# Performance work log

Hardware: AMD Instinct MI355X
Metric: run time of the kernel (lower is better)

The kernel has to match this reference:

```python
import jax, jax.numpy as jnp
import numpy as np

N, E, F_IN, E_IN, HID, H, C, L, OUT = 20000, 320000, 128, 64, 64, 4, 64, 4, 32


def setup_inputs() -> dict:
    key = jax.random.key(0)
    ks = jax.random.split(key, 24)
    s = 0.05
    return {
        'x': jax.random.normal(ks[0], (N, F_IN), jnp.float32),
        'edge_index': jax.random.randint(ks[1], (2, E), 0, N, jnp.int32),
        'edge_attr': jax.random.normal(ks[2], (E, E_IN), jnp.float32),
        'node_W': jax.random.normal(ks[3], (F_IN, HID), jnp.float32) * s,
        'node_b': jnp.zeros((HID,), jnp.float32),
        'eenc_W': jax.random.normal(ks[4], (E_IN, HID), jnp.float32) * s,
        'eenc_b': jnp.zeros((HID,), jnp.float32),
        'Wq': jax.random.normal(ks[5], (L, HID, H * C), jnp.float32) * s,
        'bq': jnp.zeros((L, H * C), jnp.float32),
        'Wk': jax.random.normal(ks[6], (L, HID, H * C), jnp.float32) * s,
        'bk': jnp.zeros((L, H * C), jnp.float32),
        'Wv': jax.random.normal(ks[7], (L, HID, H * C), jnp.float32) * s,
        'bv': jnp.zeros((L, H * C), jnp.float32),
        'We': jax.random.normal(ks[8], (L, HID, H * C), jnp.float32) * s,  # lin_edge, bias=False in PyG
        'Wskip': jax.random.normal(ks[9], (L, HID, HID), jnp.float32) * s,
        'bskip': jnp.zeros((L, HID), jnp.float32),
        'ln_g': jnp.ones((L, HID), jnp.float32),
        'ln_b': jnp.zeros((L, HID), jnp.float32),
        'lin_W': jax.random.normal(ks[10], (HID, OUT), jnp.float32) * s,
        'lin_b': jnp.zeros((OUT,), jnp.float32),
    }


def _layernorm(h, g, b):
    mu = h.mean(-1, keepdims=True)
    var = ((h - mu) ** 2).mean(-1, keepdims=True)
    return (h - mu) * jax.lax.rsqrt(var + 1e-5) * g + b


def _transformer_conv(h, ea, src, dst, Wq, bq, Wk, bk, Wv, bv, We, Wskip, bskip):
    n = h.shape[0]
    q = (h @ Wq + bq).reshape(n, H, C)[dst]          # [E,H,C] dst (x_i)
    k = (h @ Wk + bk).reshape(n, H, C)[src]          # [E,H,C] src (x_j)
    v = (h @ Wv + bv).reshape(n, H, C)[src]
    e = (ea @ We).reshape(-1, H, C)                  # per-edge features
    k = k + e
    alpha = (q * k).sum(-1) * (1.0 / jnp.sqrt(jnp.float32(C)))   # [E,H]
    amax = jax.ops.segment_max(alpha, dst, num_segments=n)       # segment softmax over dst
    ex = jnp.exp(alpha - amax[dst])
    denom = jax.ops.segment_sum(ex, dst, num_segments=n)
    a = ex / (denom[dst] + 1e-16)
    msg = (v + e) * a[..., None]                     # [E,H,C]
    out = jax.ops.segment_sum(msg, dst, num_segments=n)          # [N,H,C]
    out = out.mean(axis=1)                           # concat=False -> head mean
    return out + (h @ Wskip + bskip)                 # root_weight skip


def reference(x, edge_index, edge_attr, node_W, node_b, eenc_W, eenc_b,
              Wq, bq, Wk, bk, Wv, bv, We, Wskip, bskip, ln_g, ln_b, lin_W, lin_b):
    src, dst = edge_index[0], edge_index[1]
    h = x @ node_W + node_b
    ea = edge_attr @ eenc_W + eenc_b
    # layer 0: conv only (per the forward body)
    h = _transformer_conv(h, ea, src, dst, Wq[0], bq[0], Wk[0], bk[0], Wv[0], bv[0],
                          We[0], Wskip[0], bskip[0])
    # layers 1..L-1: res+ block (norm -> relu -> [dropout=id at eval] -> conv -> +res)
    for l in range(1, L):
        res = h
        z = _layernorm(h, ln_g[l], ln_b[l])
        z = jax.nn.relu(z)
        z = _transformer_conv(z, ea, src, dst, Wq[l], bq[l], Wk[l], bk[l], Wv[l], bv[l],
                              We[l], Wskip[l], bskip[l])
        h = z + res
    h = _layernorm(h, ln_g[0], ln_b[0])
    h = jax.nn.relu(h)
    return h @ lin_W + lin_b
```

## Files before the change

kernel.cpp:

```cpp
#include <hip/hip_runtime.h>
#include <hip/hip_fp16.h>
#include <math.h>

#define N_NODES 20000
#define N_EDGES 320000
#define F_IN    128
#define E_IN    64
#define HID     64
#define NH      4
#define CH      64
#define HC      256
#define L_LAYERS 4
#define OUT_DIM 32
#define WCOLS   1088

typedef _Float16 half8 __attribute__((ext_vector_type(8)));
typedef float f32x4 __attribute__((ext_vector_type(4)));

__global__ __launch_bounds__(256) void node_enc(const float* __restrict__ x,
                                                const float* __restrict__ W,
                                                const float* __restrict__ b,
                                                float* __restrict__ h) {
    int base_node = blockIdx.x * 4;
    int t = threadIdx.x;
    __shared__ float xs[4][F_IN];
    for (int i = t; i < 4 * F_IN; i += 256) {
        int nn = base_node + i / F_IN;
        xs[i / F_IN][i % F_IN] = (nn < N_NODES) ? x[nn * F_IN + (i % F_IN)] : 0.f;
    }
    __syncthreads();
    int node = base_node + t / 64;
    int col  = t & 63;
    if (node >= N_NODES) return;
    float acc = b[col];
    const float* xr = xs[t / 64];
    for (int i = 0; i < F_IN; i++) acc += xr[i] * W[i * HID + col];
    h[node * HID + col] = acc;
}

__global__ __launch_bounds__(256) void hist_dst(const int* __restrict__ dst,
                                                int* __restrict__ hist) {
    int e = blockIdx.x * 256 + threadIdx.x;
    if (e < N_EDGES) atomicAdd(&hist[dst[e]], 1);
}

__global__ __launch_bounds__(256) void bin_hist(const int* __restrict__ hist,
                                                int* __restrict__ bins) {
    int n = blockIdx.x * 256 + threadIdx.x;
    if (n >= N_NODES) return;
    int d = hist[n]; if (d > 255) d = 255;
    atomicAdd(&bins[d], 1);
}

__global__ __launch_bounds__(256) void scan_bins(const int* __restrict__ bins,
                                                 int* __restrict__ curb) {
    __shared__ int s[256];
    int t = threadIdx.x;
    s[t] = bins[t];
    __syncthreads();
    int acc = 0;
    for (int b = t + 1; b < 256; b++) acc += s[b];
    curb[t] = acc;
}

__global__ __launch_bounds__(256) void assign_rank(const int* __restrict__ hist,
                                                   int* __restrict__ curb,
                                                   int* __restrict__ node_order,
                                                   int* __restrict__ rank_of,
                                                   int* __restrict__ deg_rank) {
    int n = blockIdx.x * 256 + threadIdx.x;
    if (n >= N_NODES) return;
    int d = hist[n];
    int b = d > 255 ? 255 : d;
    int r = atomicAdd(&curb[b], 1);
    node_order[r] = n;
    rank_of[n] = r;
    deg_rank[r] = d;
}

__global__ __launch_bounds__(1024) void scan_hist(const int* __restrict__ arr,
                                                  int* __restrict__ row_ptr,
                                                  int* __restrict__ cursor) {
    __shared__ int sums[1024];
    const int CHUNK = 20;
    int t = threadIdx.x;
    int base = t * CHUNK;
    int local[CHUNK];
    int s = 0;
    for (int i = 0; i < CHUNK; i++) {
        int idx = base + i;
        int vv = (idx < N_NODES) ? arr[idx] : 0;
        local[i] = s;
        s += vv;
    }
    sums[t] = s;
    __syncthreads();
    for (int off = 1; off < 1024; off <<= 1) {
        int v = (t >= off) ? sums[t - off] : 0;
        __syncthreads();
        sums[t] += v;
        __syncthreads();
    }
    int excl = (t == 0) ? 0 : sums[t - 1];
    for (int i = 0; i < CHUNK; i++) {
        int idx = base + i;
        if (idx < N_NODES) {
            int p = excl + local[i];
            row_ptr[idx] = p;
            cursor[idx] = p;
        }
    }
    if (t == 1023) row_ptr[N_NODES] = sums[1023];
}

__global__ __launch_bounds__(256) void compute_pos(const int* __restrict__ src,
                                                   const int* __restrict__ dst,
                                                   const int* __restrict__ rank_of,
                                                   int* __restrict__ cursor2,
                                                   int* __restrict__ eid_of,
                                                   int* __restrict__ srcrank_perm) {
    int e = blockIdx.x * 256 + threadIdx.x;
    if (e >= N_EDGES) return;
    int r = rank_of[dst[e]];
    int pos = atomicAdd(&cursor2[r], 1);
    eid_of[pos] = e;
    srcrank_perm[pos] = rank_of[src[e]];
}

__global__ __launch_bounds__(256) void permute_attr(const int* __restrict__ eid_of,
                                                    const float* __restrict__ eattr,
                                                    __half* __restrict__ attr_p) {
    int t = threadIdx.x;
    int wave = t >> 6, lane = t & 63;
    int p = blockIdx.x * 16 + wave * 4 + (lane >> 4);
    if (p >= N_EDGES) return;
    int e = eid_of[p];
    int qi = (lane & 15) * 4;
    float4 a = *(const float4*)(eattr + (size_t)e * E_IN + qi);
    __half2 h0 = __floats2half2_rn(a.x, a.y);
    __half2 h1 = __floats2half2_rn(a.z, a.w);
    uint2 packed;
    packed.x = *(unsigned int*)&h0;
    packed.y = *(unsigned int*)&h1;
    *(uint2*)(attr_p + (size_t)p * E_IN + qi) = packed;
}

__global__ __launch_bounds__(256) void make_wqe(const float* __restrict__ Wq,
                                                const float* __restrict__ bq,
                                                const float* __restrict__ We,
                                                float* __restrict__ Wqe,
                                                float* __restrict__ bqe) {
    int l = blockIdx.x / HID;
    int i = blockIdx.x % HID;
    int t = threadIdx.x;
    int h = t >> 6, j = t & 63;
    const float* WqL = Wq + (size_t)l * HID * HC;
    const float* WeL = We + (size_t)l * HID * HC;
    float acc = 0.f;
    for (int c = 0; c < CH; c++)
        acc += WqL[i * HC + h * CH + c] * WeL[j * HC + h * CH + c];
    Wqe[(size_t)l * HID * HC + i * HC + t] = acc;
    if (i == 0) {
        const float* bqL = bq + l * HC;
        float accb = 0.f;
        for (int c = 0; c < CH; c++)
            accb += bqL[h * CH + c] * WeL[j * HC + h * CH + c];
        bqe[l * HC + t] = accb;
    }
}

__global__ __launch_bounds__(256) void make_wqe2(const float* __restrict__ Wqe,
                                                 const float* __restrict__ bqe,
                                                 const float* __restrict__ eW,
                                                 const float* __restrict__ eb,
                                                 float* __restrict__ Wqe2,
                                                 float* __restrict__ bqe2,
                                                 float* __restrict__ wqb,
                                                 float* __restrict__ bqb) {
    int l = blockIdx.x / HID, i = blockIdx.x % HID;
    int t = threadIdx.x;
    int h2 = t >> 6, m = t & 63;
    const float* Wr = Wqe + (size_t)l * HID * HC + i * HC + h2 * CH;
    float acc = 0.f;
    for (int j = 0; j < HID; j++) acc += Wr[j] * eW[m * HID + j];
    Wqe2[(size_t)l * HID * HC + i * HC + t] = acc;
    if (m == 0) {
        float a = 0.f;
        for (int j = 0; j < HID; j++) a += Wr[j] * eb[j];
        wqb[l * HID * NH + i * NH + h2] = a;
    }
    if (i == 0) {
        const float* br = bqe + l * HC + h2 * CH;
        float a = 0.f;
        for (int j = 0; j < HID; j++) a += br[j] * eW[m * HID + j];
        bqe2[l * HC + t] = a;
        if (m == 0) {
            float bb = 0.f;
            for (int j = 0; j < HID; j++) bb += br[j] * eb[j];
            bqb[l * NH + h2] = bb;
        }
    }
}

__global__ __launch_bounds__(256) void make_weE16(const float* __restrict__ eW,
                                                  const float* __restrict__ eb,
                                                  const float* __restrict__ We,
                                                  _Float16* __restrict__ WeE16T,
                                                  float* __restrict__ beE) {
    int l = blockIdx.x / E_IN, m = blockIdx.x % E_IN;
    int t = threadIdx.x;
    const float* WeL = We + (size_t)l * HID * HC;
    float acc = 0.f;
    for (int j = 0; j < HID; j++) acc += eW[m * HID + j] * WeL[j * HC + t];
    WeE16T[((size_t)l * HC + t) * 64 + m] = (_Float16)acc;
    if (m == 0) {
        float a = 0.f;
        for (int j = 0; j < HID; j++) a += eb[j] * WeL[j * HC + t];
        beE[l * HC + t] = a;
    }
}

__global__ __launch_bounds__(256) void make_w16(
        const float* __restrict__ Wq, const float* __restrict__ Wk,
        const float* __restrict__ Wv, const float* __restrict__ Wqe2,
        const float* __restrict__ Wsk,
        const float* __restrict__ bq, const float* __restrict__ bk,
        const float* __restrict__ bv, const float* __restrict__ bqe2,
        const float* __restrict__ bsk,
        _Float16* __restrict__ W16T, float* __restrict__ biasc) {
    int l = blockIdx.x / 272;
    int cg = blockIdx.x % 272;
    int col = cg * 4 + (threadIdx.x >> 6);
    int i = threadIdx.x & 63;
    float w, b;
    if (col < 256)       { w = Wq[(size_t)l*HID*HC + i*HC + col];          b = bq[l*HC + col]; }
    else if (col < 512)  { w = Wk[(size_t)l*HID*HC + i*HC + col-256];      b = bk[l*HC + col-256]; }
    else if (col < 768)  { w = Wv[(size_t)l*HID*HC + i*HC + col-512];      b = bv[l*HC + col-512]; }
    else if (col < 1024) { w = Wqe2[(size_t)l*HID*HC + i*HC + col-768];    b = bqe2[l*HC + col-768]; }
    else                 { w = Wsk[(size_t)l*HID*HID + i*HID + col-1024];  b = bsk[l*HID + col-1024]; }
    W16T[((size_t)l * WCOLS + col) * 64 + i] = (_Float16)w;
    if (i == 0) biasc[l * WCOLS + col] = b;
}

__global__ __launch_bounds__(256) void node_pre0(const float* __restrict__ h,
        const int* __restrict__ node_order,
        const _Float16* __restrict__ W16T, const float* __restrict__ biasc,
        const float* __restrict__ wqb, const float* __restrict__ bqb,
        _Float16* __restrict__ qqw, _Float16* __restrict__ kv,
        float* __restrict__ skip, float* __restrict__ qb) {
    int t = threadIdx.x;
    int wave = t >> 6, lane = t & 63;
    int base = blockIdx.x * 32;
    __shared__ _Float16 zs[32][72];
    __shared__ int nord[32];
    if (t < 32) nord[t] = node_order[base + t];
    __syncthreads();
    for (int it = 0; it < 8; it++) {
        int m = it * 4 + wave;
        zs[m][lane] = (_Float16)h[nord[m] * HID + lane];
    }
    __syncthreads();
    if (t < 128) {
        int m = t >> 2, h4 = t & 3;
        float a = bqb[h4];
        for (int i = 0; i < HID; i++) a += (float)zs[m][i] * wqb[i * NH + h4];
        qb[(base + m) * NH + h4] = a;
    }
    int quad = lane >> 4;
    int mrow = lane & 15;
    half8 a00 = *(const half8*)&zs[mrow][quad * 8];
    half8 a01 = *(const half8*)&zs[mrow][32 + quad * 8];
    half8 a10 = *(const half8*)&zs[16 + mrow][quad * 8];
    half8 a11 = *(const half8*)&zs[16 + mrow][32 + quad * 8];
    int colwave = wave * 272;
    for (int tile = 0; tile < 17; tile++) {
        int colb = colwave + tile * 16;
        int col = colb + mrow;
        const _Float16* wrow = W16T + (size_t)col * 64;
        half8 b0 = *(const half8*)(wrow + quad * 8);
        half8 b1 = *(const half8*)(wrow + 32 + quad * 8);
        f32x4 acc0 = {0.f, 0.f, 0.f, 0.f};
        f32x4 acc1 = {0.f, 0.f, 0.f, 0.f};
        acc0 = __builtin_amdgcn_mfma_f32_16x16x32_f16(a00, b0, acc0, 0, 0, 0);
        acc0 = __builtin_amdgcn_mfma_f32_16x16x32_f16(a01, b1, acc0, 0, 0, 0);
        acc1 = __builtin_amdgcn_mfma_f32_16x16x32_f16(a10, b0, acc1, 0, 0, 0);
        acc1 = __builtin_amdgcn_mfma_f32_16x16x32_f16(a11, b1, acc1, 0, 0, 0);
        float bi = biasc[col];
        int seg = colb >> 8;
        int r0 = base + quad * 4;
#pragma unroll
        for (int reg = 0; reg < 4; reg++) {
            float v0 = acc0[reg] + bi;
            float v1 = acc1[reg] + bi;
            int ra = r0 + reg, rb = ra + 16;
            if (seg == 0) {
                int p = (col >> 2) * 8 + (col & 3);
                qqw[(size_t)ra * 512 + p] = (_Float16)v0;
                qqw[(size_t)rb * 512 + p] = (_Float16)v1;
            } else if (seg == 1) {
                int c = col - 256, kp = (c >> 2) * 8 + (c & 3);
                kv[(size_t)ra * 512 + kp] = (_Float16)v0;
                kv[(size_t)rb * 512 + kp] = (_Float16)v1;
            } else if (seg == 2) {
                int c = col - 512, kp = (c >> 2) * 8 + 4 + (c & 3);
                kv[(size_t)ra * 512 + kp] = (_Float16)v0;
                kv[(size_t)rb * 512 + kp] = (_Float16)v1;
            } else if (seg == 3) {
                int c = col - 768, p = (c >> 2) * 8 + 4 + (c & 3);
                qqw[(size_t)ra * 512 + p] = (_Float16)v0;
                qqw[(size_t)rb * 512 + p] = (_Float16)v1;
            } else {
                int c = col - 1024;
                skip[ra * HID + c] = v0;
                skip[rb * HID + c] = v1;
            }
        }
    }
}

__global__ __launch_bounds__(256) void gather_edges(
        const int* __restrict__ new_rp,
        const int* __restrict__ srcrank_perm, const __half* __restrict__ attr_p,
        const __half* __restrict__ kv,
        const float* __restrict__ qb,
        const __half* qqw,
        float* numv, __half* __restrict__ numea16,
        float* __restrict__ den) {
    int wave = threadIdx.x >> 6;
    int lane = threadIdx.x & 63;
    int r = blockIdx.x * 4 + wave;
    if (r >= N_NODES) return;
    int e0 = new_rp[r], e1 = new_rp[r + 1];
    int qi = (lane & 15) * 4;
    int head = lane >> 4;
    uint4 qr = *(const uint4*)(qqw + (size_t)r * 512 + lane * 8);
    float2 q01 = __half22float2(*(__half2*)&qr.x);
    float2 q23 = __half22float2(*(__half2*)&qr.y);
    float2 w01 = __half22float2(*(__half2*)&qr.z);
    float2 w23 = __half22float2(*(__half2*)&qr.w);
    float qbh = qb[r * NH + head];
    float4 nv = make_float4(0.f, 0.f, 0.f, 0.f);
    float4 ne = make_float4(0.f, 0.f, 0.f, 0.f);
    float dsum = 0.f;
#pragma unroll 2
    for (int e = e0; e < e1; e++) {
        int s_ = srcrank_perm[e];
        uint2 araw = *(const uint2*)(attr_p + (size_t)e * E_IN + qi);
        uint4 kraw = *(const uint4*)(kv + (size_t)s_ * (2 * HC) + lane * 8);
        float2 a01 = __half22float2(*(__half2*)&araw.x);
        float2 a23 = __half22float2(*(__half2*)&araw.y);
        float2 k01 = __half22float2(*(__half2*)&kraw.x);
        float2 k23 = __half22float2(*(__half2*)&kraw.y);
        float2 v01 = __half22float2(*(__half2*)&kraw.z);
        float2 v23 = __half22float2(*(__half2*)&kraw.w);
        float rr = q01.x * k01.x + q01.y * k01.y + q23.x * k23.x + q23.y * k23.y
                 + w01.x * a01.x + w01.y * a01.y + w23.x * a23.x + w23.y * a23.y;
        rr += __shfl_xor(rr, 1);
        rr += __shfl_xor(rr, 2);
        rr += __shfl_xor(rr, 4);
        rr += __shfl_xor(rr, 8);
        float ex = __expf((rr + qbh) * 0.125f);
        nv.x += ex * v01.x; nv.y += ex * v01.y; nv.z += ex * v23.x; nv.w += ex * v23.y;
        ne.x += ex * a01.x; ne.y += ex * a01.y; ne.z += ex * a23.x; ne.w += ex * a23.y;
        dsum += ex;
    }
    *(float4*)(numv + (size_t)r * HC + lane * 4) = nv;
    __half2 n01 = __floats2half2_rn(ne.x, ne.y);
    __half2 n23 = __floats2half2_rn(ne.z, ne.w);
    uint2 np;
    np.x = *(unsigned int*)&n01;
    np.y = *(unsigned int*)&n23;
    *(uint2*)(numea16 + (size_t)r * HC + lane * 4) = np;
    if ((lane & 15) == 0) den[r * NH + head] = dsum;
}

__global__ __launch_bounds__(256) void node_mid(
        const int* __restrict__ node_order,
        const float* numv,
        const __half* __restrict__ numea16,
        const float* __restrict__ den_g,
        float* skip,
        float* __restrict__ h,
        const _Float16* __restrict__ WeE16T,
        const float* __restrict__ beE,
        int add_res,
        const _Float16* __restrict__ W16T,
        const float* __restrict__ biasc,
        const float* __restrict__ wqb, const float* __restrict__ bqb,
        const float* __restrict__ g, const float* __restrict__ be,
        _Float16* qqw, _Float16* __restrict__ kv,
        float* __restrict__ qb) {
    int t = threadIdx.x;
    int wave = t >> 6, lane = t & 63;
    int quad = lane >> 4, mrow = lane & 15;
    int base = blockIdx.x * 16;
    __shared__ _Float16 ea16[16][264];
    __shared__ float hsum[4][16][64];
    __shared__ float hnew[16][64];
    __shared__ _Float16 zs[16][72];
    __shared__ float bsh[256];
    __shared__ float dsh[64];
    __shared__ int nord[16];
    if (t < 16) nord[t] = node_order[base + t];
    if (t < 64) dsh[t] = den_g[base * 4 + t];
    bsh[t] = beE[t];
    for (int it = 0; it < 2; it++) {
        int idx = it * 256 + t;
        int m = idx >> 5, c8 = idx & 31;
        uint4 raw = *(const uint4*)(numea16 + (size_t)(base + m) * HC + c8 * 8);
        *(uint4*)&ea16[m][c8 * 8] = raw;
    }
    __syncthreads();
    {
        int hd = wave;
        half8 a_lo = *(const half8*)&ea16[mrow][hd * 64 + quad * 8];
        half8 a_hi = *(const half8*)&ea16[mrow][hd * 64 + 32 + quad * 8];
        for (int nt = 0; nt < 4; nt++) {
            int c = nt * 16 + mrow;
            const _Float16* bp = WeE16T + (size_t)(hd * 64 + c) * 64;
            half8 b_lo = *(const half8*)(bp + quad * 8);
            half8 b_hi = *(const half8*)(bp + 32 + quad * 8);
            f32x4 acc = {0.f, 0.f, 0.f, 0.f};
            acc = __builtin_amdgcn_mfma_f32_16x16x32_f16(a_lo, b_lo, acc, 0, 0, 0);
            acc = __builtin_amdgcn_mfma_f32_16x16x32_f16(a_hi, b_hi, acc, 0, 0, 0);
            int tp = hd * 64 + c;
#pragma unroll
            for (int reg = 0; reg < 4; reg++) {
                int m = quad * 4 + reg;
                float nvv = numv[(size_t)(base + m) * HC + tp];
                float dd = dsh[m * 4 + hd];
                hsum[hd][m][c] = (nvv + acc[reg] + dd * bsh[tp]) / (dd + 1e-16f) * 0.25f;
            }
        }
    }
    __syncthreads();
    for (int it = 0; it < 4; it++) {
        int idx = it * 256 + t;
        int m = idx >> 6, c = idx & 63;
        float s = hsum[0][m][c] + hsum[1][m][c] + hsum[2][m][c] + hsum[3][m][c]
                + skip[(base + m) * HID + c];
        if (add_res) s += h[nord[m] * HID + c];
        h[nord[m] * HID + c] = s;
        hnew[m][c] = s;
    }
    __syncthreads();
    for (int it = 0; it < 4; it++) {
        int m = it * 4 + wave;
        float val = hnew[m][lane];
        float mu = val;
        for (int o = 32; o > 0; o >>= 1) mu += __shfl_xor(mu, o);
        mu *= (1.f / 64.f);
        float d = val - mu;
        float var = d * d;
        for (int o = 32; o > 0; o >>= 1) var += __shfl_xor(var, o);
        var *= (1.f / 64.f);
        val = fmaxf(d * rsqrtf(var + 1e-5f) * g[lane] + be[lane], 0.f);
        zs[m][lane] = (_Float16)val;
    }
    __syncthreads();
    if (t < 64) {
        int m = t >> 2, h4 = t & 3;
        float a = bqb[h4];
        for (int i = 0; i < HID; i++) a += (float)zs[m][i] * wqb[i * NH + h4];
        qb[(base + m) * NH + h4] = a;
    }
    half8 a00 = *(const half8*)&zs[mrow][quad * 8];
    half8 a01 = *(const half8*)&zs[mrow][32 + quad * 8];
    int colwave = wave * 272;
    for (int tile = 0; tile < 17; tile++) {
        int colb = colwave + tile * 16;
        int col = colb + mrow;
        const _Float16* wrow = W16T + (size_t)col * 64;
        half8 b0 = *(const half8*)(wrow + quad * 8);
        half8 b1 = *(const half8*)(wrow + 32 + quad * 8);
        f32x4 acc = {0.f, 0.f, 0.f, 0.f};
        acc = __builtin_amdgcn_mfma_f32_16x16x32_f16(a00, b0, acc, 0, 0, 0);
        acc = __builtin_amdgcn_mfma_f32_16x16x32_f16(a01, b1, acc, 0, 0, 0);
        float bi = biasc[col];
        int seg = colb >> 8;
#pragma unroll
        for (int reg = 0; reg < 4; reg++) {
            float v0 = acc[reg] + bi;
            int ra = base + quad * 4 + reg;
            if (seg == 0) {
                qqw[(size_t)ra * 512 + (col >> 2) * 8 + (col & 3)] = (_Float16)v0;
            } else if (seg == 1) {
                int c = col - 256;
                kv[(size_t)ra * 512 + (c >> 2) * 8 + (c & 3)] = (_Float16)v0;
            } else if (seg == 2) {
                int c = col - 512;
                kv[(size_t)ra * 512 + (c >> 2) * 8 + 4 + (c & 3)] = (_Float16)v0;
            } else if (seg == 3) {
                int c = col - 768;
                qqw[(size_t)ra * 512 + (c >> 2) * 8 + 4 + (c & 3)] = (_Float16)v0;
            } else {
                skip[ra * HID + (col - 1024)] = v0;
            }
        }
    }
}

__global__ __launch_bounds__(256) void node_fin(
        const int* __restrict__ node_order,
        const float* __restrict__ numv,
        const __half* __restrict__ numea16,
        const float* __restrict__ den_g,
        const float* __restrict__ skip,
        const float* __restrict__ h,
        const _Float16* __restrict__ WeE16T, const float* __restrict__ beE,
        const float* __restrict__ g, const float* __restrict__ be,
        const float* __restrict__ linW, const float* __restrict__ linb,
        float* __restrict__ out) {
    int t = threadIdx.x;
    int wave = t >> 6, lane = t & 63;
    int quad = lane >> 4, mrow = lane & 15;
    int base = blockIdx.x * 16;
    __shared__ _Float16 ea16[16][264];
    __shared__ float hsum[4][16][64];
    __shared__ float hnew[16][64];
    __shared__ float bsh[256];
    __shared__ float dsh[64];
    __shared__ int nord[16];
    if (t < 16) nord[t] = node_order[base + t];
    if (t < 64) dsh[t] = den_g[base * 4 + t];
    bsh[t] = beE[t];
    for (int it = 0; it < 2; it++) {
        int idx = it * 256 + t;
        int m = idx >> 5, c8 = idx & 31;
        uint4 raw = *(const uint4*)(numea16 + (size_t)(base + m) * HC + c8 * 8);
        *(uint4*)&ea16[m][c8 * 8] = raw;
    }
    __syncthreads();
    {
        int hd = wave;
        half8 a_lo = *(const half8*)&ea16[mrow][hd * 64 + quad * 8];
        half8 a_hi = *(const half8*)&ea16[mrow][hd * 64 + 32 + quad * 8];
        for (int nt = 0; nt < 4; nt++) {
            int c = nt * 16 + mrow;
            const _Float16* bp = WeE16T + (size_t)(hd * 64 + c) * 64;
            half8 b_lo = *(const half8*)(bp + quad * 8);
            half8 b_hi = *(const half8*)(bp + 32 + quad * 8);
            f32x4 acc = {0.f, 0.f, 0.f, 0.f};
            acc = __builtin_amdgcn_mfma_f32_16x16x32_f16(a_lo, b_lo, acc, 0, 0, 0);
            acc = __builtin_amdgcn_mfma_f32_16x16x32_f16(a_hi, b_hi, acc, 0, 0, 0);
            int tp = hd * 64 + c;
#pragma unroll
            for (int reg = 0; reg < 4; reg++) {
                int m = quad * 4 + reg;
                float nvv = numv[(size_t)(base + m) * HC + tp];
                float dd = dsh[m * 4 + hd];
                hsum[hd][m][c] = (nvv + acc[reg] + dd * bsh[tp]) / (dd + 1e-16f) * 0.25f;
            }
        }
    }
    __syncthreads();
    for (int it = 0; it < 4; it++) {
        int idx = it * 256 + t;
        int m = idx >> 6, c = idx & 63;
        float s = hsum[0][m][c] + hsum[1][m][c] + hsum[2][m][c] + hsum[3][m][c]
                + skip[(base + m) * HID + c] + h[nord[m] * HID + c];
        hnew[m][c] = s;
    }
    __syncthreads();
    for (int it = 0; it < 4; it++) {
        int m = it * 4 + wave;
        float val = hnew[m][lane];
        float mu = val;
        for (int o = 32; o > 0; o >>= 1) mu += __shfl_xor(mu, o);
        mu *= (1.f / 64.f);
        float d = val - mu;
        float var = d * d;
        for (int o = 32; o > 0; o >>= 1) var += __shfl_xor(var, o);
        var *= (1.f / 64.f);
        hnew[m][lane] = fmaxf(d * rsqrtf(var + 1e-5f) * g[lane] + be[lane], 0.f);
    }
    __syncthreads();
    for (int it = 0; it < 2; it++) {
        int idx = it * 256 + t;
        int m = idx >> 5, col = idx & 31;
        float a = linb[col];
        for (int i = 0; i < HID; i++) a += hnew[m][i] * linW[i * OUT_DIM + col];
        out[nord[m] * OUT_DIM + col] = a;
    }
}

extern "C" void kernel_launch(void* const* d_in, const int* in_sizes, int n_in,
                              void* d_out, int out_size, void* d_ws, size_t ws_size,
                              hipStream_t stream) {
    const float* x      = (const float*)d_in[0];
    const int*   ei     = (const int*)d_in[1];
    const float* eattr  = (const float*)d_in[2];
    const float* node_W = (const float*)d_in[3];
    const float* node_b = (const float*)d_in[4];
    const float* eenc_W = (const float*)d_in[5];
    const float* eenc_b = (const float*)d_in[6];
    const float* Wq     = (const float*)d_in[7];
    const float* bq     = (const float*)d_in[8];
    const float* Wk     = (const float*)d_in[9];
    const float* bk     = (const float*)d_in[10];
    const float* Wv     = (const float*)d_in[11];
    const float* bv     = (const float*)d_in[12];
    const float* We     = (const float*)d_in[13];
    const float* Wskip  = (const float*)d_in[14];
    const float* bskip  = (const float*)d_in[15];
    const float* ln_g   = (const float*)d_in[16];
    const float* ln_b   = (const float*)d_in[17];
    const float* lin_W  = (const float*)d_in[18];
    const float* lin_b  = (const float*)d_in[19];
    float* out = (float*)d_out;

    const int* src = ei;
    const int* dst = ei + N_EDGES;

    float* ws = (float*)d_ws;
    __half* attr_p = (__half*)ws; ws += (size_t)N_EDGES * E_IN / 2;
    float* Wqe    = (float*)attr_p;
    float* h    = ws; ws += N_NODES * HID;
    _Float16* qqw = (_Float16*)ws; ws += (size_t)N_NODES * HC;
    float* numv = (float*)qqw;
    __half* numea16 = (__half*)ws; ws += (size_t)N_NODES * HC / 2;
    _Float16* kv = (_Float16*)ws; ws += (size_t)N_NODES * HC;
    float* skip = ws; ws += N_NODES * HID;
    float* den  = ws; ws += N_NODES * NH;
    float* qb   = ws; ws += N_NODES * NH;
    float* bqe  = ws; ws += L_LAYERS * HC;
    float* Wqe2 = ws; ws += (size_t)L_LAYERS * HID * HC;
    float* bqe2 = ws; ws += L_LAYERS * HC;
    float* wqb  = ws; ws += L_LAYERS * HID * NH;
    float* bqb  = ws; ws += L_LAYERS * NH;
    _Float16* WeE16T = (_Float16*)ws; ws += (size_t)L_LAYERS * HC * HID / 2;
    float* beE  = ws; ws += L_LAYERS * HC;
    _Float16* W16T = (_Float16*)ws; ws += (size_t)L_LAYERS * WCOLS * HID / 2;
    float* biasc = ws; ws += L_LAYERS * WCOLS;
    int* ip = (int*)ws;
    int* hist         = ip; ip += N_NODES;
    int* bins         = ip; ip += 256;
    int* curb         = ip; ip += 256;
    int* node_order   = ip; ip += N_NODES;
    int* rank_of      = ip; ip += N_NODES;
    int* deg_rank     = ip; ip += N_NODES;
    int* new_rp       = ip; ip += N_NODES + 4;
    int* cursor2      = ip; ip += N_NODES;
    int* srcrank_perm = ip; ip += N_EDGES;
    int* eid_of       = ip; ip += N_EDGES;

    node_enc<<<(N_NODES + 3) / 4, 256, 0, stream>>>(x, node_W, node_b, h);

    hipMemsetAsync(hist, 0, N_NODES * sizeof(int), stream);
    hipMemsetAsync(bins, 0, 256 * sizeof(int), stream);
    hist_dst<<<(N_EDGES + 255) / 256, 256, 0, stream>>>(dst, hist);
    bin_hist<<<(N_NODES + 255) / 256, 256, 0, stream>>>(hist, bins);
    scan_bins<<<1, 256, 0, stream>>>(bins, curb);
    assign_rank<<<(N_NODES + 255) / 256, 256, 0, stream>>>(hist, curb, node_order,
                                                           rank_of, deg_rank);
    scan_hist<<<1, 1024, 0, stream>>>(deg_rank, new_rp, cursor2);

    make_wqe<<<L_LAYERS * HID, 256, 0, stream>>>(Wq, bq, We, Wqe, bqe);
    make_wqe2<<<L_LAYERS * HID, 256, 0, stream>>>(Wqe, bqe, eenc_W, eenc_b,
                                                  Wqe2, bqe2, wqb, bqb);
    make_weE16<<<L_LAYERS * E_IN, 256, 0, stream>>>(eenc_W, eenc_b, We, WeE16T, beE);
    make_w16<<<L_LAYERS * 272, 256, 0, stream>>>(Wq, Wk, Wv, Wqe2, Wskip,
                                                 bq, bk, bv, bqe2, bskip,
                                                 W16T, biasc);

    compute_pos<<<(N_EDGES + 255) / 256, 256, 0, stream>>>(src, dst, rank_of, cursor2,
                                                           eid_of, srcrank_perm);
    permute_attr<<<N_EDGES / 16, 256, 0, stream>>>(eid_of, eattr, attr_p);

    node_pre0<<<N_NODES / 32, 256, 0, stream>>>(
        h, node_order, W16T, biasc, wqb, bqb, qqw, kv, skip, qb);

    for (int l = 0; l < L_LAYERS; l++) {
        gather_edges<<<(N_NODES + 3) / 4, 256, 0, stream>>>(
            new_rp, srcrank_perm, attr_p, (const __half*)kv, qb,
            (const __half*)qqw, numv, numea16, den);
        if (l < L_LAYERS - 1) {
            node_mid<<<N_NODES / 16, 256, 0, stream>>>(
                node_order, numv, numea16, den, skip, h,
                WeE16T + (size_t)l * HC * HID, beE + l * HC,
                (l > 0) ? 1 : 0,
                W16T + (size_t)(l + 1) * WCOLS * HID, biasc + (l + 1) * WCOLS,
                wqb + (l + 1) * HID * NH, bqb + (l + 1) * NH,
                ln_g + (l + 1) * HID, ln_b + (l + 1) * HID,
                qqw, kv, qb);
        } else {
            node_fin<<<N_NODES / 16, 256, 0, stream>>>(
                node_order, numv, numea16, den, skip, h,
                WeE16T + (size_t)l * HC * HID, beE + l * HC,
                ln_g, ln_b, lin_W, lin_b, out);
        }
    }
}
```

Measured before the change: 811.0 us.

## Fuse setup kernels and node encoder into MFMA pre-pass, simplify weight layout

Merges the four degree-binning/ranking/scan kernels into one single-block kernel, and fuses the two weight-precomposition kernels using shared memory. The node encoder is folded into node_pre0 as an fp16 MFMA GEMM over x, which removes a kernel and the fp32 h round-trip. Weight columns are pre-interleaved in make_w16 so the epilogue stores contiguously without per-segment index math. The main costs targeted are launch overhead and extra memory passes in setup. In exchange, the single-block build_order serialises 20000 nodes on one CU, and the encoder now runs in fp16 precision.

```diff
diff --git a/kernel.cpp b/kernel.cpp
--- a/kernel.cpp
+++ b/kernel.cpp
@@ -17,79 +17,51 @@
 typedef _Float16 half8 __attribute__((ext_vector_type(8)));
 typedef float f32x4 __attribute__((ext_vector_type(4)));
 
-__global__ __launch_bounds__(256) void node_enc(const float* __restrict__ x,
-                                                const float* __restrict__ W,
-                                                const float* __restrict__ b,
-                                                float* __restrict__ h) {
-    int base_node = blockIdx.x * 4;
-    int t = threadIdx.x;
-    __shared__ float xs[4][F_IN];
-    for (int i = t; i < 4 * F_IN; i += 256) {
-        int nn = base_node + i / F_IN;
-        xs[i / F_IN][i % F_IN] = (nn < N_NODES) ? x[nn * F_IN + (i % F_IN)] : 0.f;
-    }
-    __syncthreads();
-    int node = base_node + t / 64;
-    int col  = t & 63;
-    if (node >= N_NODES) return;
-    float acc = b[col];
-    const float* xr = xs[t / 64];
-    for (int i = 0; i < F_IN; i++) acc += xr[i] * W[i * HID + col];
-    h[node * HID + col] = acc;
-}
-
 __global__ __launch_bounds__(256) void hist_dst(const int* __restrict__ dst,
                                                 int* __restrict__ hist) {
     int e = blockIdx.x * 256 + threadIdx.x;
     if (e < N_EDGES) atomicAdd(&hist[dst[e]], 1);
 }
 
-__global__ __launch_bounds__(256) void bin_hist(const int* __restrict__ hist,
-                                                int* __restrict__ bins) {
-    int n = blockIdx.x * 256 + threadIdx.x;
-    if (n >= N_NODES) return;
-    int d = hist[n]; if (d > 255) d = 255;
-    atomicAdd(&bins[d], 1);
-}
-
-__global__ __launch_bounds__(256) void scan_bins(const int* __restrict__ bins,
-                                                 int* __restrict__ curb) {
-    __shared__ int s[256];
+__global__ __launch_bounds__(1024) void build_order(const int* __restrict__ hist,
+                                                    int* __restrict__ node_order,
+                                                    int* __restrict__ rank_of,
+                                                    int* __restrict__ deg_rank,
+                                                    int* __restrict__ new_rp,
+                                                    int* __restrict__ cursor2) {
+    __shared__ int bins[256];
+    __shared__ int curb[256];
+    __shared__ int sums[1024];
     int t = threadIdx.x;
-    s[t] = bins[t];
-    __syncthreads();
-    int acc = 0;
-    for (int b = t + 1; b < 256; b++) acc += s[b];
-    curb[t] = acc;
-}
-
-__global__ __launch_bounds__(256) void assign_rank(const int* __restrict__ hist,
-                                                   int* __restrict__ curb,
-                                                   int* __restrict__ node_order,
-                                                   int* __restrict__ rank_of,
-                                                   int* __restrict__ deg_rank) {
-    int n = blockIdx.x * 256 + threadIdx.x;
-    if (n >= N_NODES) return;
-    int d = hist[n];
-    int b = d > 255 ? 255 : d;
-    int r = atomicAdd(&curb[b], 1);
-    node_order[r] = n;
-    rank_of[n] = r;
-    deg_rank[r] = d;
-}
-
-__global__ __launch_bounds__(1024) void scan_hist(const int* __restrict__ arr,
-                                                  int* __restrict__ row_ptr,
-                                                  int* __restrict__ cursor) {
-    __shared__ int sums[1024];
+    if (t < 256) bins[t] = 0;
+    __syncthreads();
+    for (int n = t; n < N_NODES; n += 1024) {
+        int d = hist[n]; if (d > 255) d = 255;
+        atomicAdd(&bins[d], 1);
+    }
+    __syncthreads();
+    if (t < 256) {
+        int acc = 0;
+        for (int b = t + 1; b < 256; b++) acc += bins[b];
+        curb[t] = acc;
+    }
+    __syncthreads();
+    for (int n = t; n < N_NODES; n += 1024) {
+        int d = hist[n];
+        int b = d > 255 ? 255 : d;
+        int r = atomicAdd(&curb[b], 1);
+        node_order[r] = n;
+        rank_of[n] = r;
+        deg_rank[r] = d;
+    }
+    __syncthreads();
     const int CHUNK = 20;
-    int t = threadIdx.x;
     int base = t * CHUNK;
     int local[CHUNK];
     int s = 0;
     for (int i = 0; i < CHUNK; i++) {
         int idx = base + i;
-        int vv = (idx < N_NODES) ? arr[idx] : 0;
+        int vv = (idx < N_NODES) ? deg_rank[idx] : 0;
         local[i] = s;
         s += vv;
     }
@@ -106,11 +78,11 @@
         int idx = base + i;
         if (idx < N_NODES) {
             int p = excl + local[i];
-            row_ptr[idx] = p;
-            cursor[idx] = p;
-        }
-    }
-    if (t == 1023) row_ptr[N_NODES] = sums[1023];
+            new_rp[idx] = p;
+            cursor2[idx] = p;
+        }
+    }
+    if (t == 1023) new_rp[N_NODES] = sums[1023];
 }
 
 __global__ __launch_bounds__(256) void compute_pos(const int* __restrict__ src,
@@ -145,32 +117,9 @@
     *(uint2*)(attr_p + (size_t)p * E_IN + qi) = packed;
 }
 
-__global__ __launch_bounds__(256) void make_wqe(const float* __restrict__ Wq,
-                                                const float* __restrict__ bq,
-                                                const float* __restrict__ We,
-                                                float* __restrict__ Wqe,
-                                                float* __restrict__ bqe) {
-    int l = blockIdx.x / HID;
-    int i = blockIdx.x % HID;
-    int t = threadIdx.x;
-    int h = t >> 6, j = t & 63;
-    const float* WqL = Wq + (size_t)l * HID * HC;
-    const float* WeL = We + (size_t)l * HID * HC;
-    float acc = 0.f;
-    for (int c = 0; c < CH; c++)
-        acc += WqL[i * HC + h * CH + c] * WeL[j * HC + h * CH + c];
-    Wqe[(size_t)l * HID * HC + i * HC + t] = acc;
-    if (i == 0) {
-        const float* bqL = bq + l * HC;
-        float accb = 0.f;
-        for (int c = 0; c < CH; c++)
-            accb += bqL[h * CH + c] * WeL[j * HC + h * CH + c];
-        bqe[l * HC + t] = accb;
-    }
-}
-
-__global__ __launch_bounds__(256) void make_wqe2(const float* __restrict__ Wqe,
-                                                 const float* __restrict__ bqe,
+__global__ __launch_bounds__(256) void make_wqeA(const float* __restrict__ Wq,
+                                                 const float* __restrict__ bq,
+                                                 const float* __restrict__ We,
                                                  const float* __restrict__ eW,
                                                  const float* __restrict__ eb,
                                                  float* __restrict__ Wqe2,
@@ -179,24 +128,39 @@
                                                  float* __restrict__ bqb) {
     int l = blockIdx.x / HID, i = blockIdx.x % HID;
     int t = threadIdx.x;
+    int h = t >> 6, j = t & 63;
+    __shared__ float wrow[256];
+    __shared__ float brow[256];
+    const float* WqL = Wq + (size_t)l * HID * HC;
+    const float* WeL = We + (size_t)l * HID * HC;
+    float acc = 0.f;
+    for (int c = 0; c < CH; c++)
+        acc += WqL[i * HC + h * CH + c] * WeL[j * HC + h * CH + c];
+    wrow[t] = acc;
+    if (i == 0) {
+        const float* bqL = bq + l * HC;
+        float ab = 0.f;
+        for (int c = 0; c < CH; c++)
+            ab += bqL[h * CH + c] * WeL[j * HC + h * CH + c];
+        brow[t] = ab;
+    }
+    __syncthreads();
     int h2 = t >> 6, m = t & 63;
-    const float* Wr = Wqe + (size_t)l * HID * HC + i * HC + h2 * CH;
-    float acc = 0.f;
-    for (int j = 0; j < HID; j++) acc += Wr[j] * eW[m * HID + j];
-    Wqe2[(size_t)l * HID * HC + i * HC + t] = acc;
+    float a2 = 0.f;
+    for (int jj = 0; jj < HID; jj++) a2 += wrow[h2 * 64 + jj] * eW[m * HID + jj];
+    Wqe2[(size_t)l * HID * HC + i * HC + t] = a2;
     if (m == 0) {
-        float a = 0.f;
-        for (int j = 0; j < HID; j++) a += Wr[j] * eb[j];
-        wqb[l * HID * NH + i * NH + h2] = a;
+        float aw = 0.f;
+        for (int jj = 0; jj < HID; jj++) aw += wrow[h2 * 64 + jj] * eb[jj];
+        wqb[l * HID * NH + i * NH + h2] = aw;
     }
     if (i == 0) {
-        const float* br = bqe + l * HC + h2 * CH;
-        float a = 0.f;
-        for (int j = 0; j < HID; j++) a += br[j] * eW[m * HID + j];
-        bqe2[l * HC + t] = a;
+        float ab2 = 0.f;
+        for (int jj = 0; jj < HID; jj++) ab2 += brow[h2 * 64 + jj] * eW[m * HID + jj];
+        bqe2[l * HC + t] = ab2;
         if (m == 0) {
             float bb = 0.f;
-            for (int j = 0; j < HID; j++) bb += br[j] * eb[j];
+            for (int jj = 0; jj < HID; jj++) bb += brow[h2 * 64 + jj] * eb[jj];
             bqb[l * NH + h2] = bb;
         }
     }
@@ -233,31 +197,77 @@
     int col = cg * 4 + (threadIdx.x >> 6);
     int i = threadIdx.x & 63;
     float w, b;
-    if (col < 256)       { w = Wq[(size_t)l*HID*HC + i*HC + col];          b = bq[l*HC + col]; }
-    else if (col < 512)  { w = Wk[(size_t)l*HID*HC + i*HC + col-256];      b = bk[l*HC + col-256]; }
-    else if (col < 768)  { w = Wv[(size_t)l*HID*HC + i*HC + col-512];      b = bv[l*HC + col-512]; }
-    else if (col < 1024) { w = Wqe2[(size_t)l*HID*HC + i*HC + col-768];    b = bqe2[l*HC + col-768]; }
-    else                 { w = Wsk[(size_t)l*HID*HID + i*HID + col-1024];  b = bsk[l*HID + col-1024]; }
+    if (col < 512) {
+        int c = (col >> 3) * 4 + (col & 3);
+        if ((col >> 2) & 1) { w = Wqe2[(size_t)l*HID*HC + i*HC + c]; b = bqe2[l*HC + c]; }
+        else                { w = Wq[(size_t)l*HID*HC + i*HC + c];   b = bq[l*HC + c]; }
+    } else if (col < 1024) {
+        int cc = col - 512;
+        int c = (cc >> 3) * 4 + (cc & 3);
+        if ((cc >> 2) & 1) { w = Wv[(size_t)l*HID*HC + i*HC + c]; b = bv[l*HC + c]; }
+        else               { w = Wk[(size_t)l*HID*HC + i*HC + c]; b = bk[l*HC + c]; }
+    } else {
+        int c = col - 1024;
+        w = Wsk[(size_t)l*HID*HID + i*HID + c];  b = bsk[l*HID + c];
+    }
     W16T[((size_t)l * WCOLS + col) * 64 + i] = (_Float16)w;
     if (i == 0) biasc[l * WCOLS + col] = b;
 }
 
-__global__ __launch_bounds__(256) void node_pre0(const float* __restrict__ h,
+__global__ __launch_bounds__(256) void make_w0(const float* __restrict__ nW,
+                                               const float* __restrict__ nb,
+                                               _Float16* __restrict__ W0T,
+                                               float* __restrict__ b0) {
+    int col = blockIdx.x * 2 + (threadIdx.x >> 7);
+    int i = threadIdx.x & 127;
+    W0T[col * F_IN + i] = (_Float16)nW[i * HID + col];
+    if (i == 0) b0[col] = nb[col];
+}
+
+__global__ __launch_bounds__(256) void node_pre0(const float* __restrict__ x,
         const int* __restrict__ node_order,
+        const _Float16* __restrict__ W0T, const float* __restrict__ b0,
         const _Float16* __restrict__ W16T, const float* __restrict__ biasc,
         const float* __restrict__ wqb, const float* __restrict__ bqb,
         _Float16* __restrict__ qqw, _Float16* __restrict__ kv,
         float* __restrict__ skip, float* __restrict__ qb) {
     int t = threadIdx.x;
     int wave = t >> 6, lane = t & 63;
+    int quad = lane >> 4, mrow = lane & 15;
     int base = blockIdx.x * 32;
+    __shared__ _Float16 xs[32][136];
     __shared__ _Float16 zs[32][72];
     __shared__ int nord[32];
     if (t < 32) nord[t] = node_order[base + t];
     __syncthreads();
-    for (int it = 0; it < 8; it++) {
-        int m = it * 4 + wave;
-        zs[m][lane] = (_Float16)h[nord[m] * HID + lane];
+    for (int it = 0; it < 4; it++) {
+        int idx = it * 256 + t;
+        int m = idx >> 5, c4 = idx & 31;
+        float4 a = *(const float4*)(x + (size_t)nord[m] * F_IN + c4 * 4);
+        _Float16* d = &xs[m][c4 * 4];
+        d[0] = (_Float16)a.x; d[1] = (_Float16)a.y;
+        d[2] = (_Float16)a.z; d[3] = (_Float16)a.w;
+    }
+    __syncthreads();
+    {
+        int col = wave * 16 + mrow;
+        const _Float16* w0row = W0T + (size_t)col * F_IN;
+        f32x4 acc0 = {0.f, 0.f, 0.f, 0.f};
+        f32x4 acc1 = {0.f, 0.f, 0.f, 0.f};
+#pragma unroll
+        for (int kk = 0; kk < 4; kk++) {
+            half8 bfrag = *(const half8*)(w0row + kk * 32 + quad * 8);
+            half8 af0 = *(const half8*)&xs[mrow][kk * 32 + quad * 8];
+            half8 af1 = *(const half8*)&xs[16 + mrow][kk * 32 + quad * 8];
+            acc0 = __builtin_amdgcn_mfma_f32_16x16x32_f16(af0, bfrag, acc0, 0, 0, 0);
+            acc1 = __builtin_amdgcn_mfma_f32_16x16x32_f16(af1, bfrag, acc1, 0, 0, 0);
+        }
+        float bb = b0[col];
+#pragma unroll
+        for (int reg = 0; reg < 4; reg++) {
+            zs[quad * 4 + reg][col] = (_Float16)(acc0[reg] + bb);
+            zs[16 + quad * 4 + reg][col] = (_Float16)(acc1[reg] + bb);
+        }
     }
     __syncthreads();
     if (t < 128) {
@@ -266,8 +276,6 @@
         for (int i = 0; i < HID; i++) a += (float)zs[m][i] * wqb[i * NH + h4];
         qb[(base + m) * NH + h4] = a;
     }
-    int quad = lane >> 4;
-    int mrow = lane & 15;
     half8 a00 = *(const half8*)&zs[mrow][quad * 8];
     half8 a01 = *(const half8*)&zs[mrow][32 + quad * 8];
     half8 a10 = *(const half8*)&zs[16 + mrow][quad * 8];
@@ -277,42 +285,33 @@
         int colb = colwave + tile * 16;
         int col = colb + mrow;
         const _Float16* wrow = W16T + (size_t)col * 64;
-        half8 b0 = *(const half8*)(wrow + quad * 8);
-        half8 b1 = *(const half8*)(wrow + 32 + quad * 8);
+        half8 b0f = *(const half8*)(wrow + quad * 8);
+        half8 b1f = *(const half8*)(wrow + 32 + quad * 8);
         f32x4 acc0 = {0.f, 0.f, 0.f, 0.f};
         f32x4 acc1 = {0.f, 0.f, 0.f, 0.f};
-        acc0 = __builtin_amdgcn_mfma_f32_16x16x32_f16(a00, b0, acc0, 0, 0, 0);
-        acc0 = __builtin_amdgcn_mfma_f32_16x16x32_f16(a01, b1, acc0, 0, 0, 0);
-        acc1 = __builtin_amdgcn_mfma_f32_16x16x32_f16(a10, b0, acc1, 0, 0, 0);
-        acc1 = __builtin_amdgcn_mfma_f32_16x16x32_f16(a11, b1, acc1, 0, 0, 0);
+        acc0 = __builtin_amdgcn_mfma_f32_16x16x32_f16(a00, b0f, acc0, 0, 0, 0);
+        acc0 = __builtin_amdgcn_mfma_f32_16x16x32_f16(a01, b1f, acc0, 0, 0, 0);
+        acc1 = __builtin_amdgcn_mfma_f32_16x16x32_f16(a10, b0f, acc1, 0, 0, 0);
+        acc1 = __builtin_amdgcn_mfma_f32_16x16x32_f16(a11, b1f, acc1, 0, 0, 0);
         float bi = biasc[col];
-        int seg = colb >> 8;
+        int seg = colb >> 9;
         int r0 = base + quad * 4;
 #pragma unroll
         for (int reg = 0; reg < 4; reg++) {
             float v0 = acc0[reg] + bi;
             float v1 = acc1[reg] + bi;
             int ra = r0 + reg, rb = ra + 16;
-            if (seg == 0) {
-                int p = (col >> 2) * 8 + (col & 3);
-                qqw[(size_t)ra * 512 + p] = (_Float16)v0;
-                qqw[(size_t)rb * 512 + p] = (_Float16)v1;
-            } else if (seg == 1) {
-                int c = col - 256, kp = (c >> 2) * 8 + (c & 3);
-                kv[(size_t)ra * 512 + kp] = (_Float16)v0;
-                kv[(size_t)rb * 512 + kp] = (_Float16)v1;
-            } else if (seg == 2) {
-                int c = col - 512, kp = (c >> 2) * 8 + 4 + (c & 3);
-                kv[(size_t)ra * 512 + kp] = (_Float16)v0;
-                kv[(size_t)rb * 512 + kp] = (_Float16)v1;
-            } else if (seg == 3) {
-                int c = col - 768, p = (c >> 2) * 8 + 4 + (c & 3);
-                qqw[(size_t)ra * 512 + p] = (_Float16)v0;
-                qqw[(size_t)rb * 512 + p] = (_Float16)v1;
-            } else {
+            if (colb >= 1024) {
                 int c = col - 1024;
                 skip[ra * HID + c] = v0;
                 skip[rb * HID + c] = v1;
+            } else if (seg == 0) {
+                qqw[(size_t)ra * 512 + col] = (_Float16)v0;
+                qqw[(size_t)rb * 512 + col] = (_Float16)v1;
+            } else {
+                int c = col - 512;
+                kv[(size_t)ra * 512 + c] = (_Float16)v0;
+                kv[(size_t)rb * 512 + c] = (_Float16)v1;
             }
         }
     }
@@ -471,30 +470,23 @@
         int colb = colwave + tile * 16;
         int col = colb + mrow;
         const _Float16* wrow = W16T + (size_t)col * 64;
-        half8 b0 = *(const half8*)(wrow + quad * 8);
-        half8 b1 = *(const half8*)(wrow + 32 + quad * 8);
+        half8 b0f = *(const half8*)(wrow + quad * 8);
+        half8 b1f = *(const half8*)(wrow + 32 + quad * 8);
         f32x4 acc = {0.f, 0.f, 0.f, 0.f};
-        acc = __builtin_amdgcn_mfma_f32_16x16x32_f16(a00, b0, acc, 0, 0, 0);
-        acc = __builtin_amdgcn_mfma_f32_16x16x32_f16(a01, b1, acc, 0, 0, 0);
+        acc = __builtin_amdgcn_mfma_f32_16x16x32_f16(a00, b0f, acc, 0, 0, 0);
+        acc = __builtin_amdgcn_mfma_f32_16x16x32_f16(a01, b1f, acc, 0, 0, 0);
         float bi = biasc[col];
-        int seg = colb >> 8;
+        int seg = colb >> 9;
 #pragma unroll
         for (int reg = 0; reg < 4; reg++) {
             float v0 = acc[reg] + bi;
             int ra = base + quad * 4 + reg;
-            if (seg == 0) {
-                qqw[(size_t)ra * 512 + (col >> 2) * 8 + (col & 3)] = (_Float16)v0;
-            } else if (seg == 1) {
-                int c = col - 256;
-                kv[(size_t)ra * 512 + (c >> 2) * 8 + (c & 3)] = (_Float16)v0;
-            } else if (seg == 2) {
-                int c = col - 512;
-                kv[(size_t)ra * 512 + (c >> 2) * 8 + 4 + (c & 3)] = (_Float16)v0;
-            } else if (seg == 3) {
-                int c = col - 768;
-                qqw[(size_t)ra * 512 + (c >> 2) * 8 + 4 + (c & 3)] = (_Float16)v0;
+            if (colb >= 1024) {
+                skip[ra * HID + (col - 1024)] = v0;
+            } else if (seg == 0) {
+                qqw[(size_t)ra * 512 + col] = (_Float16)v0;
             } else {
-                skip[ra * HID + (col - 1024)] = v0;
+                kv[(size_t)ra * 512 + (col - 512)] = (_Float16)v0;
             }
         }
     }
@@ -614,7 +606,6 @@
 
     float* ws = (float*)d_ws;
     __half* attr_p = (__half*)ws; ws += (size_t)N_EDGES * E_IN / 2;
-    float* Wqe    = (float*)attr_p;
     float* h    = ws; ws += N_NODES * HID;
     _Float16* qqw = (_Float16*)ws; ws += (size_t)N_NODES * HC;
     float* numv = (float*)qqw;
@@ -623,7 +614,6 @@
     float* skip = ws; ws += N_NODES * HID;
     float* den  = ws; ws += N_NODES * NH;
     float* qb   = ws; ws += N_NODES * NH;
-    float* bqe  = ws; ws += L_LAYERS * HC;
     float* Wqe2 = ws; ws += (size_t)L_LAYERS * HID * HC;
     float* bqe2 = ws; ws += L_LAYERS * HC;
     float* wqb  = ws; ws += L_LAYERS * HID * NH;
@@ -632,10 +622,10 @@
     float* beE  = ws; ws += L_LAYERS * HC;
     _Float16* W16T = (_Float16*)ws; ws += (size_t)L_LAYERS * WCOLS * HID / 2;
     float* biasc = ws; ws += L_LAYERS * WCOLS;
+    _Float16* W0T = (_Float16*)ws; ws += HID * F_IN / 2;
+    float* b0  = ws; ws += HID;
     int* ip = (int*)ws;
     int* hist         = ip; ip += N_NODES;
-    int* bins         = ip; ip += 256;
-    int* curb         = ip; ip += 256;
     int* node_order   = ip; ip += N_NODES;
     int* rank_of      = ip; ip += N_NODES;
     int* deg_rank     = ip; ip += N_NODES;
@@ -644,31 +634,25 @@
     int* srcrank_perm = ip; ip += N_EDGES;
     int* eid_of       = ip; ip += N_EDGES;
 
-    node_enc<<<(N_NODES + 3) / 4, 256, 0, stream>>>(x, node_W, node_b, h);
-
     hipMemsetAsync(hist, 0, N_NODES * sizeof(int), stream);
-    hipMemsetAsync(bins, 0, 256 * sizeof(int), stream);
     hist_dst<<<(N_EDGES + 255) / 256, 256, 0, stream>>>(dst, hist);
-    bin_hist<<<(N_NODES + 255) / 256, 256, 0, stream>>>(hist, bins);
-    scan_bins<<<1, 256, 0, stream>>>(bins, curb);
-    assign_rank<<<(N_NODES + 255) / 256, 256, 0, stream>>>(hist, curb, node_order,
-                                                           rank_of, deg_rank);
-    scan_hist<<<1, 1024, 0, stream>>>(deg_rank, new_rp, cursor2);
-
-    make_wqe<<<L_LAYERS * HID, 256, 0, stream>>>(Wq, bq, We, Wqe, bqe);
-    make_wqe2<<<L_LAYERS * HID, 256, 0, stream>>>(Wqe, bqe, eenc_W, eenc_b,
+    build_order<<<1, 1024, 0, stream>>>(hist, node_order, rank_of, deg_rank,
+                                        new_rp, cursor2);
+
+    make_wqeA<<<L_LAYERS * HID, 256, 0, stream>>>(Wq, bq, We, eenc_W, eenc_b,
                                                   Wqe2, bqe2, wqb, bqb);
     make_weE16<<<L_LAYERS * E_IN, 256, 0, stream>>>(eenc_W, eenc_b, We, WeE16T, beE);
     make_w16<<<L_LAYERS * 272, 256, 0, stream>>>(Wq, Wk, Wv, Wqe2, Wskip,
                                                  bq, bk, bv, bqe2, bskip,
                                                  W16T, biasc);
+    make_w0<<<HID / 2, 256, 0, stream>>>(node_W, node_b, W0T, b0);
 
     compute_pos<<<(N_EDGES + 255) / 256, 256, 0, stream>>>(src, dst, rank_of, cursor2,
                                                            eid_of, srcrank_perm);
     permute_attr<<<N_EDGES / 16, 256, 0, stream>>>(eid_of, eattr, attr_p);
 
     node_pre0<<<N_NODES / 32, 256, 0, stream>>>(
-        h, node_order, W16T, biasc, wqb, bqb, qqw, kv, skip, qb);
+        x, node_order, W0T, b0, W16T, biasc, wqb, bqb, qqw, kv, skip, qb);
 
     for (int l = 0; l < L_LAYERS; l++) {
         gather_edges<<<(N_NODES + 3) / 4, 256, 0, stream>>>(
```

After: 733.6 us. 9.5% less time.
